# Optimization experiments

Measured on AMD Instinct MI355X. Metric: run time of the kernel, lower is better.

## Reference

```python
import jax, jax.numpy as jnp
import numpy as np

D_MODEL, D_SLOT, D_HIDDEN = 256, 256, 128


def setup_inputs() -> dict:
    key = jax.random.key(0)
    k1, k2, k3, k4, k5, k6 = jax.random.split(key, 6)
    B, T, N = 8, 1024, 64
    features = jax.random.normal(k1, (B, T, D_MODEL), dtype=jnp.float32)
    slots = jax.random.normal(k2, (B, N, D_SLOT), dtype=jnp.float32)
    # nn.Linear-style init (uniform +- 1/sqrt(fan_in))
    lim1 = 1.0 / np.sqrt(D_MODEL + D_SLOT)
    W_proj = jax.random.uniform(k3, (D_MODEL + D_SLOT, D_HIDDEN), minval=-lim1, maxval=lim1, dtype=jnp.float32)
    b_proj = jax.random.uniform(k4, (D_HIDDEN,), minval=-lim1, maxval=lim1, dtype=jnp.float32)
    lim2 = 1.0 / np.sqrt(D_HIDDEN)
    w_head = jax.random.uniform(k5, (D_HIDDEN,), minval=-lim2, maxval=lim2, dtype=jnp.float32)
    b_head = jax.random.uniform(k6, (), minval=-lim2, maxval=lim2, dtype=jnp.float32)
    return {"features": features, "slots": slots, "W_proj": W_proj, "b_proj": b_proj, "w_head": w_head, "b_head": b_head}


def reference(features, slots, W_proj, b_proj, w_head, b_head):
    # proj(concat([feat, slot])) is separable: feat @ W_f + slot @ W_s + b
    W_f = W_proj[:D_MODEL]   # (D, H)
    W_s = W_proj[D_MODEL:]   # (S, H)
    f_proj = jnp.einsum('btd,dh->bth', features, W_f)          # (B, T, H)
    s_proj = jnp.einsum('bns,sh->bnh', slots, W_s) + b_proj    # (B, N, H)
    x = jax.nn.relu(f_proj[:, :, None, :] + s_proj[:, None, :, :])  # (B, T, N, H)
    out = jnp.einsum('btnh,h->btn', x, w_head) + b_head         # (B, T, N)
    return out
```

## Files before the change

### kernel.cpp

```cpp
#include <hip/hip_runtime.h>
#include <hip/hip_bf16.h>
#include <hip/hip_fp16.h>

typedef unsigned short ushort_t;
typedef unsigned int uint_t;
typedef __attribute__((ext_vector_type(8))) short short8;
typedef __attribute__((ext_vector_type(4))) float f32x4;
typedef __attribute__((ext_vector_type(4))) unsigned int uint4v;
typedef __attribute__((ext_vector_type(2))) _Float16 half2v;

#if defined(__has_builtin)
#if __has_builtin(__builtin_amdgcn_fdot2)
#define HAVE_FDOT2 1
#endif
#endif

__device__ __forceinline__ ushort_t f2bf(float f) {
    unsigned v;
    __builtin_memcpy(&v, &f, 4);
    unsigned r = (v + 0x7FFFu + ((v >> 16) & 1u)) >> 16;
    return (ushort_t)r;
}

__global__ __launch_bounds__(1024) void asd_k1(
        const float* __restrict__ slots,
        const float* __restrict__ Wproj,
        const float* __restrict__ bproj,
        ushort_t* __restrict__ s2,
        ushort_t* __restrict__ Wpack) {
    int bid = blockIdx.x;
    int tid = threadIdx.x;
    if (bid < 256) {
        __shared__ float sl[512];
        __shared__ float part[3][256];
        int b  = bid >> 5;
        int n0 = (bid & 31) * 2;
        const float* srow = slots + (b * 64 + n0) * 256;
        if (tid < 256) {
            float2 v = ((const float2*)srow)[tid];
            sl[2 * tid]     = v.x;
            sl[2 * tid + 1] = v.y;
        }
        __syncthreads();
        int dh = tid >> 8;
        int nl = (tid >> 7) & 1;
        int h  = tid & 127;
        const float* Wcol = Wproj + 256 * 128 + dh * 64 * 128 + h;
        const float* sr   = sl + nl * 256 + dh * 64;
        float acc = 0.f;
        #pragma unroll 8
        for (int d = 0; d < 64; ++d)
            acc += sr[d] * Wcol[d * 128];
        if (dh) part[dh - 1][nl * 128 + h] = acc;
        __syncthreads();
        if (dh == 0) {
            float v = acc + part[0][nl * 128 + h] + part[1][nl * 128 + h]
                          + part[2][nl * 128 + h] + bproj[h];
            _Float16 hv = (_Float16)v;
            ushort_t u;
            __builtin_memcpy(&u, &hv, 2);
            int n = n0 + nl;
            s2[b * 8192 + (h >> 1) * 128 + n * 2 + (h & 1)] = u;
        }
    } else {
        int gid = (bid - 256) * 1024 + tid;
        int l   = gid & 63;
        int idx = gid >> 6;
        int kb  = idx >> 3, nt = idx & 7;
        int r0  = kb * 32 + ((l >> 4) << 3);
        int c   = nt * 16 + (l & 15);
        short8 frag;
        #pragma unroll
        for (int i = 0; i < 8; ++i)
            frag[i] = (short)f2bf(Wproj[(r0 + i) * 128 + c]);
        ((short8*)Wpack)[gid] = frag;
    }
}

__global__ __launch_bounds__(256) void asd_k2(
        const float* __restrict__ feat,
        const ushort_t* __restrict__ s2g,
        const ushort_t* __restrict__ Wpack,
        const float* __restrict__ whead,
        const float* __restrict__ bhead,
        float* __restrict__ out) {
    __shared__ uint_t   s2_lds[64 * 68];
    __shared__ ushort_t f_lds[16 * 132];
    __shared__ uint_t   w2_lds[64];

    int tid = threadIdx.x;
    int bid = blockIdx.x;
    int b   = bid >> 6;
    int t0  = (bid & 63) << 4;

    if (tid < 64) {
        half2v w2 = { (_Float16)whead[2 * tid], (_Float16)whead[2 * tid + 1] };
        uint_t u;
        __builtin_memcpy(&u, &w2, 4);
        w2_lds[tid] = u;
    }
    const uint4v* src = (const uint4v*)(s2g + b * 8192);
    #pragma unroll
    for (int r = 0; r < 4; ++r) {
        int i4 = r * 256 + tid;
        int h2 = i4 >> 4, c = i4 & 15;
        *(uint4v*)(s2_lds + h2 * 68 + c * 4) = src[i4];
    }
    float bh = bhead[0];

    int l = tid & 63;
    int w = tid >> 6;
    int m = l & 15, q = l >> 4;
    int nt0 = 2 * w;
    f32x4 acc0 = {0.f, 0.f, 0.f, 0.f};
    f32x4 acc1 = {0.f, 0.f, 0.f, 0.f};
    const short8* Wp = (const short8*)Wpack;
    #pragma unroll
    for (int kb = 0; kb < 8; ++kb) {
        const float* arow = feat + (b * 1024 + t0 + m) * 256 + kb * 32 + q * 8;
        f32x4 af0 = *(const f32x4*)arow;
        f32x4 af1 = *(const f32x4*)(arow + 4);
        __hip_bfloat162 c0 = __float22bfloat162_rn(make_float2(af0[0], af0[1]));
        __hip_bfloat162 c1 = __float22bfloat162_rn(make_float2(af0[2], af0[3]));
        __hip_bfloat162 c2 = __float22bfloat162_rn(make_float2(af1[0], af1[1]));
        __hip_bfloat162 c3 = __float22bfloat162_rn(make_float2(af1[2], af1[3]));
        uint_t u0, u1, u2, u3;
        __builtin_memcpy(&u0, &c0, 4);
        __builtin_memcpy(&u1, &c1, 4);
        __builtin_memcpy(&u2, &c2, 4);
        __builtin_memcpy(&u3, &c3, 4);
        uint4v au = {u0, u1, u2, u3};
        short8 A;
        __builtin_memcpy(&A, &au, 16);
        short8 B0 = Wp[(kb * 8 + nt0) * 64 + l];
        short8 B1 = Wp[(kb * 8 + nt0 + 1) * 64 + l];
        acc0 = __builtin_amdgcn_mfma_f32_16x16x32_bf16(A, B0, acc0, 0, 0, 0);
        acc1 = __builtin_amdgcn_mfma_f32_16x16x32_bf16(A, B1, acc1, 0, 0, 0);
    }
    #pragma unroll
    for (int r = 0; r < 4; ++r) {
        int row = q * 4 + r;
        _Float16 v0 = (_Float16)acc0[r];
        _Float16 v1 = (_Float16)acc1[r];
        ushort_t u0, u1;
        __builtin_memcpy(&u0, &v0, 2);
        __builtin_memcpy(&u1, &v1, 2);
        f_lds[row * 132 + nt0 * 16 + m]       = u0;
        f_lds[row * 132 + (nt0 + 1) * 16 + m] = u1;
    }
    __syncthreads();

    int t = tid >> 4, ng = tid & 15;
    const ushort_t* fR = f_lds + t * 132;
    float a0 = bh, a1 = bh, a2 = bh, a3 = bh;
    const half2v hz = { (_Float16)0.f, (_Float16)0.f };
    #pragma unroll 8
    for (int h2 = 0; h2 < 64; ++h2) {
        uint_t fu = *(const uint_t*)(fR + 2 * h2);
        half2v f2;
        __builtin_memcpy(&f2, &fu, 4);
        uint4v s4 = *(const uint4v*)(s2_lds + h2 * 68 + 4 * ng);
        uint_t wu = w2_lds[h2];
        half2v w2;
        __builtin_memcpy(&w2, &wu, 4);
        float* accs[4] = {&a0, &a1, &a2, &a3};
        #pragma unroll
        for (int j = 0; j < 4; ++j) {
            uint_t su = s4[j];
            half2v sv;
            __builtin_memcpy(&sv, &su, 4);
            half2v x = f2 + sv;
            x = __builtin_elementwise_max(x, hz);
#ifdef HAVE_FDOT2
            *accs[j] = __builtin_amdgcn_fdot2(x, w2, *accs[j], false);
#else
            *accs[j] += (float)x[0] * (float)w2[0] + (float)x[1] * (float)w2[1];
#endif
        }
    }
    f32x4 o = {a0, a1, a2, a3};
    *(f32x4*)(out + (b * 1024 + t0 + t) * 64 + 4 * ng) = o;
}

extern "C" void kernel_launch(void* const* d_in, const int* in_sizes, int n_in,
                              void* d_out, int out_size, void* d_ws, size_t ws_size,
                              hipStream_t stream) {
    const float* feat  = (const float*)d_in[0];
    const float* slots = (const float*)d_in[1];
    const float* Wproj = (const float*)d_in[2];
    const float* bproj = (const float*)d_in[3];
    const float* whead = (const float*)d_in[4];
    const float* bhead = (const float*)d_in[5];
    float* out = (float*)d_out;

    ushort_t* s2    = (ushort_t*)d_ws;
    ushort_t* Wpack = (ushort_t*)((char*)d_ws + 131072);

    hipLaunchKernelGGL(asd_k1, dim3(260), dim3(1024), 0, stream,
                       slots, Wproj, bproj, s2, Wpack);
    hipLaunchKernelGGL(asd_k2, dim3(512), dim3(256), 0, stream,
                       feat, s2, Wpack, whead, bhead, out);
}
```

Baseline: 79.08 us.

## Fuse slot projection and weight packing into single kernel with fp16 MFMA

Merges the two launches into one kernel. Each block now recomputes the per-batch slot projection (64x256 @ 256x128) with fp16 MFMA from slots staged in LDS, and builds weight fragments directly from fp32 Wproj instead of a prepacked workspace. This removes one kernel launch and the global round-trip for s2 and Wpack. The price is redundant slot-projection work in all 64 blocks per batch, strided uncoalesced weight loads, and a larger LDS footprint that may lower occupancy. It also switches bf16 to fp16 and uses round-toward-zero packing, which changes precision.

```diff
diff --git a/kernel.cpp b/kernel.cpp
--- a/kernel.cpp
+++ b/kernel.cpp
@@ -1,13 +1,13 @@
 #include <hip/hip_runtime.h>
-#include <hip/hip_bf16.h>
 #include <hip/hip_fp16.h>
 
 typedef unsigned short ushort_t;
 typedef unsigned int uint_t;
-typedef __attribute__((ext_vector_type(8))) short short8;
 typedef __attribute__((ext_vector_type(4))) float f32x4;
 typedef __attribute__((ext_vector_type(4))) unsigned int uint4v;
 typedef __attribute__((ext_vector_type(2))) _Float16 half2v;
+typedef __attribute__((ext_vector_type(2))) __fp16 fp16x2;
+typedef __attribute__((ext_vector_type(8))) _Float16 half8;
 
 #if defined(__has_builtin)
 #if __has_builtin(__builtin_amdgcn_fdot2)
@@ -15,78 +15,40 @@
 #endif
 #endif
 
-__device__ __forceinline__ ushort_t f2bf(float f) {
-    unsigned v;
-    __builtin_memcpy(&v, &f, 4);
-    unsigned r = (v + 0x7FFFu + ((v >> 16) & 1u)) >> 16;
-    return (ushort_t)r;
-}
-
-__global__ __launch_bounds__(1024) void asd_k1(
+union H8 {
+    uint4v u4;
+    half8  h8;
+    half2v h2[4];
+};
+
+__device__ __forceinline__ half2v cvt_pkrtz(float a, float b) {
+    fp16x2 r = __builtin_amdgcn_cvt_pkrtz(a, b);
+    half2v o;
+    __builtin_memcpy(&o, &r, 4);
+    return o;
+}
+
+__device__ __forceinline__ half8 wfrag(const float* __restrict__ p) {
+    H8 u;
+    u.h2[0] = cvt_pkrtz(p[0],   p[128]);
+    u.h2[1] = cvt_pkrtz(p[256], p[384]);
+    u.h2[2] = cvt_pkrtz(p[512], p[640]);
+    u.h2[3] = cvt_pkrtz(p[768], p[896]);
+    return u.h8;
+}
+
+__global__ __launch_bounds__(256) void asd_fused(
+        const float* __restrict__ feat,
         const float* __restrict__ slots,
         const float* __restrict__ Wproj,
         const float* __restrict__ bproj,
-        ushort_t* __restrict__ s2,
-        ushort_t* __restrict__ Wpack) {
-    int bid = blockIdx.x;
-    int tid = threadIdx.x;
-    if (bid < 256) {
-        __shared__ float sl[512];
-        __shared__ float part[3][256];
-        int b  = bid >> 5;
-        int n0 = (bid & 31) * 2;
-        const float* srow = slots + (b * 64 + n0) * 256;
-        if (tid < 256) {
-            float2 v = ((const float2*)srow)[tid];
-            sl[2 * tid]     = v.x;
-            sl[2 * tid + 1] = v.y;
-        }
-        __syncthreads();
-        int dh = tid >> 8;
-        int nl = (tid >> 7) & 1;
-        int h  = tid & 127;
-        const float* Wcol = Wproj + 256 * 128 + dh * 64 * 128 + h;
-        const float* sr   = sl + nl * 256 + dh * 64;
-        float acc = 0.f;
-        #pragma unroll 8
-        for (int d = 0; d < 64; ++d)
-            acc += sr[d] * Wcol[d * 128];
-        if (dh) part[dh - 1][nl * 128 + h] = acc;
-        __syncthreads();
-        if (dh == 0) {
-            float v = acc + part[0][nl * 128 + h] + part[1][nl * 128 + h]
-                          + part[2][nl * 128 + h] + bproj[h];
-            _Float16 hv = (_Float16)v;
-            ushort_t u;
-            __builtin_memcpy(&u, &hv, 2);
-            int n = n0 + nl;
-            s2[b * 8192 + (h >> 1) * 128 + n * 2 + (h & 1)] = u;
-        }
-    } else {
-        int gid = (bid - 256) * 1024 + tid;
-        int l   = gid & 63;
-        int idx = gid >> 6;
-        int kb  = idx >> 3, nt = idx & 7;
-        int r0  = kb * 32 + ((l >> 4) << 3);
-        int c   = nt * 16 + (l & 15);
-        short8 frag;
-        #pragma unroll
-        for (int i = 0; i < 8; ++i)
-            frag[i] = (short)f2bf(Wproj[(r0 + i) * 128 + c]);
-        ((short8*)Wpack)[gid] = frag;
-    }
-}
-
-__global__ __launch_bounds__(256) void asd_k2(
-        const float* __restrict__ feat,
-        const ushort_t* __restrict__ s2g,
-        const ushort_t* __restrict__ Wpack,
         const float* __restrict__ whead,
         const float* __restrict__ bhead,
         float* __restrict__ out) {
-    __shared__ uint_t   s2_lds[64 * 68];
-    __shared__ ushort_t f_lds[16 * 132];
-    __shared__ uint_t   w2_lds[64];
+    __shared__ __attribute__((aligned(16))) ushort_t sl_lds[64 * 264];
+    __shared__ __attribute__((aligned(16))) uint_t   s2_lds[64 * 68];
+    __shared__ __attribute__((aligned(16))) ushort_t f_lds[16 * 136];
+    __shared__ __attribute__((aligned(16))) uint_t   w2_lds[64];
 
     int tid = threadIdx.x;
     int bid = blockIdx.x;
@@ -94,48 +56,53 @@
     int t0  = (bid & 63) << 4;
 
     if (tid < 64) {
-        half2v w2 = { (_Float16)whead[2 * tid], (_Float16)whead[2 * tid + 1] };
+        half2v wv = cvt_pkrtz(whead[2 * tid], whead[2 * tid + 1]);
         uint_t u;
-        __builtin_memcpy(&u, &w2, 4);
+        __builtin_memcpy(&u, &wv, 4);
         w2_lds[tid] = u;
     }
-    const uint4v* src = (const uint4v*)(s2g + b * 8192);
-    #pragma unroll
-    for (int r = 0; r < 4; ++r) {
-        int i4 = r * 256 + tid;
-        int h2 = i4 >> 4, c = i4 & 15;
-        *(uint4v*)(s2_lds + h2 * 68 + c * 4) = src[i4];
-    }
-    float bh = bhead[0];
-
-    int l = tid & 63;
-    int w = tid >> 6;
+
+    {
+        const float* sb = slots + b * (64 * 256);
+        #pragma unroll
+        for (int k = 0; k < 8; ++k) {
+            int g = k * 256 + tid;
+            int r = g >> 5, c = g & 31;
+            const f32x4* src = (const f32x4*)(sb + r * 256 + c * 8);
+            f32x4 v0 = src[0];
+            f32x4 v1 = src[1];
+            H8 u;
+            u.h2[0] = cvt_pkrtz(v0[0], v0[1]);
+            u.h2[1] = cvt_pkrtz(v0[2], v0[3]);
+            u.h2[2] = cvt_pkrtz(v1[0], v1[1]);
+            u.h2[3] = cvt_pkrtz(v1[2], v1[3]);
+            *(uint4v*)((char*)sl_lds + r * 528 + c * 16) = u.u4;
+        }
+    }
+
+    int l = tid & 63, w = tid >> 6;
     int m = l & 15, q = l >> 4;
     int nt0 = 2 * w;
+    int c0 = nt0 * 16 + m;
+    int c1 = c0 + 16;
+
     f32x4 acc0 = {0.f, 0.f, 0.f, 0.f};
     f32x4 acc1 = {0.f, 0.f, 0.f, 0.f};
-    const short8* Wp = (const short8*)Wpack;
-    #pragma unroll
+    #pragma unroll 2
     for (int kb = 0; kb < 8; ++kb) {
         const float* arow = feat + (b * 1024 + t0 + m) * 256 + kb * 32 + q * 8;
         f32x4 af0 = *(const f32x4*)arow;
         f32x4 af1 = *(const f32x4*)(arow + 4);
-        __hip_bfloat162 c0 = __float22bfloat162_rn(make_float2(af0[0], af0[1]));
-        __hip_bfloat162 c1 = __float22bfloat162_rn(make_float2(af0[2], af0[3]));
-        __hip_bfloat162 c2 = __float22bfloat162_rn(make_float2(af1[0], af1[1]));
-        __hip_bfloat162 c3 = __float22bfloat162_rn(make_float2(af1[2], af1[3]));
-        uint_t u0, u1, u2, u3;
-        __builtin_memcpy(&u0, &c0, 4);
-        __builtin_memcpy(&u1, &c1, 4);
-        __builtin_memcpy(&u2, &c2, 4);
-        __builtin_memcpy(&u3, &c3, 4);
-        uint4v au = {u0, u1, u2, u3};
-        short8 A;
-        __builtin_memcpy(&A, &au, 16);
-        short8 B0 = Wp[(kb * 8 + nt0) * 64 + l];
-        short8 B1 = Wp[(kb * 8 + nt0 + 1) * 64 + l];
-        acc0 = __builtin_amdgcn_mfma_f32_16x16x32_bf16(A, B0, acc0, 0, 0, 0);
-        acc1 = __builtin_amdgcn_mfma_f32_16x16x32_bf16(A, B1, acc1, 0, 0, 0);
+        H8 A;
+        A.h2[0] = cvt_pkrtz(af0[0], af0[1]);
+        A.h2[1] = cvt_pkrtz(af0[2], af0[3]);
+        A.h2[2] = cvt_pkrtz(af1[0], af1[1]);
+        A.h2[3] = cvt_pkrtz(af1[2], af1[3]);
+        const float* wp = Wproj + (kb * 32 + q * 8) * 128;
+        half8 B0 = wfrag(wp + c0);
+        half8 B1 = wfrag(wp + c1);
+        acc0 = __builtin_amdgcn_mfma_f32_16x16x32_f16(A.h8, B0, acc0, 0, 0, 0);
+        acc1 = __builtin_amdgcn_mfma_f32_16x16x32_f16(A.h8, B1, acc1, 0, 0, 0);
     }
     #pragma unroll
     for (int r = 0; r < 4; ++r) {
@@ -145,37 +112,85 @@
         ushort_t u0, u1;
         __builtin_memcpy(&u0, &v0, 2);
         __builtin_memcpy(&u1, &v1, 2);
-        f_lds[row * 132 + nt0 * 16 + m]       = u0;
-        f_lds[row * 132 + (nt0 + 1) * 16 + m] = u1;
+        f_lds[row * 136 + c0] = u0;
+        f_lds[row * 136 + c1] = u1;
     }
     __syncthreads();
 
+    f32x4 sa[4][2];
+    #pragma unroll
+    for (int mt = 0; mt < 4; ++mt) {
+        sa[mt][0] = (f32x4){0.f, 0.f, 0.f, 0.f};
+        sa[mt][1] = (f32x4){0.f, 0.f, 0.f, 0.f};
+    }
+    const float* Ws = Wproj + 256 * 128;
+    #pragma unroll 2
+    for (int kb = 0; kb < 8; ++kb) {
+        const float* wp = Ws + (kb * 32 + q * 8) * 128;
+        half8 B0 = wfrag(wp + c0);
+        half8 B1 = wfrag(wp + c1);
+        #pragma unroll
+        for (int mt = 0; mt < 4; ++mt) {
+            half8 As = *(const half8*)((const char*)sl_lds +
+                        (mt * 16 + m) * 528 + kb * 64 + q * 16);
+            sa[mt][0] = __builtin_amdgcn_mfma_f32_16x16x32_f16(As, B0, sa[mt][0], 0, 0, 0);
+            sa[mt][1] = __builtin_amdgcn_mfma_f32_16x16x32_f16(As, B1, sa[mt][1], 0, 0, 0);
+        }
+    }
+    {
+        float bp0 = bproj[c0];
+        float bp1 = bproj[c1];
+        ushort_t* s2s = (ushort_t*)s2_lds;
+        int h2a = c0 >> 1, pa = c0 & 1;
+        int h2b = c1 >> 1, pb = c1 & 1;
+        #pragma unroll
+        for (int mt = 0; mt < 4; ++mt) {
+            #pragma unroll
+            for (int r = 0; r < 4; ++r) {
+                int n = mt * 16 + q * 4 + r;
+                _Float16 v0 = (_Float16)(sa[mt][0][r] + bp0);
+                _Float16 v1 = (_Float16)(sa[mt][1][r] + bp1);
+                ushort_t u0, u1;
+                __builtin_memcpy(&u0, &v0, 2);
+                __builtin_memcpy(&u1, &v1, 2);
+                s2s[h2a * 136 + n * 2 + pa] = u0;
+                s2s[h2b * 136 + n * 2 + pb] = u1;
+            }
+        }
+    }
+    __syncthreads();
+
     int t = tid >> 4, ng = tid & 15;
-    const ushort_t* fR = f_lds + t * 132;
+    const ushort_t* fR = f_lds + t * 136;
+    float bh = bhead[0];
     float a0 = bh, a1 = bh, a2 = bh, a3 = bh;
-    const half2v hz = { (_Float16)0.f, (_Float16)0.f };
-    #pragma unroll 8
-    for (int h2 = 0; h2 < 64; ++h2) {
-        uint_t fu = *(const uint_t*)(fR + 2 * h2);
-        half2v f2;
-        __builtin_memcpy(&f2, &fu, 4);
-        uint4v s4 = *(const uint4v*)(s2_lds + h2 * 68 + 4 * ng);
-        uint_t wu = w2_lds[h2];
-        half2v w2;
-        __builtin_memcpy(&w2, &wu, 4);
-        float* accs[4] = {&a0, &a1, &a2, &a3};
+    const half2v hz = {(_Float16)0.f, (_Float16)0.f};
+    #pragma unroll 4
+    for (int g = 0; g < 16; ++g) {
+        uint4v f4 = *(const uint4v*)(fR + g * 8);
+        uint4v w4 = *(const uint4v*)(w2_lds + g * 4);
         #pragma unroll
         for (int j = 0; j < 4; ++j) {
-            uint_t su = s4[j];
-            half2v sv;
-            __builtin_memcpy(&sv, &su, 4);
-            half2v x = f2 + sv;
-            x = __builtin_elementwise_max(x, hz);
+            int h2 = g * 4 + j;
+            uint_t fu = f4[j], wu = w4[j];
+            half2v f2, wv;
+            __builtin_memcpy(&f2, &fu, 4);
+            __builtin_memcpy(&wv, &wu, 4);
+            uint4v s4 = *(const uint4v*)(s2_lds + h2 * 68 + 4 * ng);
+            float* accs[4] = {&a0, &a1, &a2, &a3};
+            #pragma unroll
+            for (int j2 = 0; j2 < 4; ++j2) {
+                uint_t su = s4[j2];
+                half2v sv;
+                __builtin_memcpy(&sv, &su, 4);
+                half2v x = f2 + sv;
+                x = __builtin_elementwise_max(x, hz);
 #ifdef HAVE_FDOT2
-            *accs[j] = __builtin_amdgcn_fdot2(x, w2, *accs[j], false);
+                *accs[j2] = __builtin_amdgcn_fdot2(x, wv, *accs[j2], false);
 #else
-            *accs[j] += (float)x[0] * (float)w2[0] + (float)x[1] * (float)w2[1];
+                *accs[j2] += (float)x[0] * (float)wv[0] + (float)x[1] * (float)wv[1];
 #endif
+            }
         }
     }
     f32x4 o = {a0, a1, a2, a3};
@@ -193,11 +208,6 @@
     const float* bhead = (const float*)d_in[5];
     float* out = (float*)d_out;
 
-    ushort_t* s2    = (ushort_t*)d_ws;
-    ushort_t* Wpack = (ushort_t*)((char*)d_ws + 131072);
-
-    hipLaunchKernelGGL(asd_k1, dim3(260), dim3(1024), 0, stream,
-                       slots, Wproj, bproj, s2, Wpack);
-    hipLaunchKernelGGL(asd_k2, dim3(512), dim3(256), 0, stream,
-                       feat, s2, Wpack, whead, bhead, out);
-}
+    hipLaunchKernelGGL(asd_fused, dim3(512), dim3(256), 0, stream,
+                       feat, slots, Wproj, bproj, whead, bhead, out);
+}
```

Result: no change. 80.65 us, median of 2 (+2.0%).
